# Kernel optimization log

Hardware: AMD Instinct MI355X
Metric: run time of the kernel (lower is better)

## Reference

```python
import jax, jax.numpy as jnp
import numpy as np

N, MA, F, NF = 512, 64, 128, 16
UPDATE_RATIO = 0.1
DECAY = 1.0
EPS = 1e-12  # avoids NaN grad of sqrt at self-distance 0 (torch diagonal is masked out by exp anyway)


def setup_inputs() -> dict:
    key = jax.random.key(0)
    ks = jax.random.split(key, 8)
    z = jax.random.randint(ks[0], (N, MA), 0, 10, dtype=jnp.int64) if jax.config.jax_enable_x64 else jax.random.randint(ks[0], (N, MA), 0, 10, dtype=jnp.int32)
    # pad last few atoms of each molecule with -1 to exercise the mask
    z = z.at[:, MA - 8:].set(-1)
    r = jax.random.normal(ks[1], (N, MA, 3), dtype=jnp.float32) * 3.0
    h = jax.random.normal(ks[2], (N, MA, F), dtype=jnp.float32)
    distances = jnp.linspace(0.5, 6.0, NF, dtype=jnp.float32)
    widths = jax.random.uniform(ks[3], (NF,), dtype=jnp.float32) * 0.5 + 0.5  # keep sigma > 0
    din = F * (1 + NF)  # 2176
    W1 = jax.random.normal(ks[4], (din, 512), dtype=jnp.float32) * (1.0 / np.sqrt(din))
    b1 = jnp.zeros((512,), dtype=jnp.float32)
    W2 = jax.random.normal(ks[5], (512, F), dtype=jnp.float32) * (1.0 / np.sqrt(512.0))
    b2 = jnp.zeros((F,), dtype=jnp.float32)
    return {"z": z, "r": r, "h": h, "distances": distances, "widths": widths,
            "W1": W1, "b1": b1, "W2": W2, "b2": b2}


def reference(z, r, h, distances, widths, W1, b1, W2, b2):
    n, ma = z.shape
    nf = distances.shape[0]
    # pairwise distance: (n, ma, ma)
    dv = r[:, :, None, :] - r[:, None, :, :]
    d = jnp.sqrt(jnp.sum(dv * dv, axis=-1) + EPS)
    mu = distances.reshape(1, nf, 1, 1)
    sigma = widths.reshape(1, nf, 1, 1)
    mask1 = (z > -1).astype(h.dtype)                      # (n, ma)
    pair_mask = mask1[:, :, None] * mask1[:, None, :]     # (n, ma, ma)
    # Gaussian RBF scores, masked: (n, nf, ma, ma)
    w = pair_mask[:, None] * jnp.exp(-((d[:, None] - mu) ** 2) / sigma) * 5.0
    # aggregate neighbor features: (n, ma, nf, F) -> (n, ma, nf*F)
    u = jnp.einsum('nfab,nbc->nafc', w, h).reshape(n, ma, nf * h.shape[-1])
    v = jnp.concatenate([h, u], axis=2)                   # (n, ma, F*(1+nf))
    v = jax.nn.silu(v @ W1 + b1) @ W2 + b2                # MLP 'net'
    h_new = h + v * UPDATE_RATIO * DECAY * mask1[:, :, None]
    return (z, r, h_new)
```

## Files before the change

### kernel.cpp

```cpp
#include <hip/hip_runtime.h>

#define MA 64
#define F 128
#define NF 16
#define HID 512
#define LDUB 144
#define LDWB 144
#define LDT1B 1040
#define UB0 0
#define UB1 9216
#define WL0 18432
#define WL1 27648

typedef float  float4v __attribute__((ext_vector_type(4)));
typedef short  short8  __attribute__((ext_vector_type(8)));
typedef int    int8v   __attribute__((ext_vector_type(8)));

static __device__ __forceinline__ unsigned int pack2bf(float x, float y) {
    unsigned int a = __float_as_uint(x) + 0x8000u;
    unsigned int b = __float_as_uint(y) + 0x8000u;
    return __builtin_amdgcn_perm(b, a, 0x07060302u);
}
static __device__ __forceinline__ unsigned short f2bf1(float x) {
    return (unsigned short)((__float_as_uint(x) + 0x8000u) >> 16);
}
static __device__ __forceinline__ unsigned int pk4fp8(float a, float b, float c, float d) {
    int p = __builtin_amdgcn_cvt_pk_fp8_f32(a, b, 0, false);
    p = __builtin_amdgcn_cvt_pk_fp8_f32(c, d, p, true);
    return (unsigned int)p;
}

#define LGKM_BAR() do {                                        \
    asm volatile("s_waitcnt lgkmcnt(0)" ::: "memory");         \
    __builtin_amdgcn_s_barrier();                              \
    asm volatile("" ::: "memory");                             \
} while (0)

__global__ void pack_frags(const float* __restrict__ W1, const float* __restrict__ W2,
                           unsigned char* __restrict__ w1p, unsigned short* __restrict__ w2p) {
    int gid  = blockIdx.x * 4 + (threadIdx.x >> 6);
    int lane = threadIdx.x & 63;
    int arow = lane & 15;
    int kq   = lane >> 4;
    if (gid < 544) {
        int kt = gid >> 5, jt = gid & 31;
        const float* base = W1 + (size_t)(kt * 128 + kq * 32) * HID + jt * 16 + arow;
        unsigned int o[8];
        #pragma unroll
        for (int p = 0; p < 8; p++)
            o[p] = pk4fp8(base[(p * 4 + 0) * HID], base[(p * 4 + 1) * HID],
                          base[(p * 4 + 2) * HID], base[(p * 4 + 3) * HID]);
        unsigned char* dst = w1p + ((size_t)gid * 64 + lane) * 32;
        *(uint4*)dst        = (uint4){o[0], o[1], o[2], o[3]};
        *(uint4*)(dst + 16) = (uint4){o[4], o[5], o[6], o[7]};
    } else if (gid < 544 + 128) {
        int g2 = gid - 544;
        int kt = g2 >> 3, mt = g2 & 7;
        const float* base = W2 + (size_t)(kt * 32 + kq * 8) * F + mt * 16 + arow;
        short8 o;
        #pragma unroll
        for (int j = 0; j < 8; j++) o[j] = (short)f2bf1(base[j * F]);
        *(short8*)(w2p + ((size_t)g2 * 64 + lane) * 8) = o;
    }
}

__launch_bounds__(512, 4)
__global__ void node_conv_mfma(const int* __restrict__ z, const float* __restrict__ rr,
        const float* __restrict__ h, const float* __restrict__ dist,
        const float* __restrict__ wid, const float* __restrict__ b1,
        const float* __restrict__ b2,
        const unsigned char* __restrict__ w1p, const unsigned short* __restrict__ w2p,
        float* __restrict__ out) {
    const int n = blockIdx.x;
    const int tid = threadIdx.x;
    const int lane = tid & 63;
    const int wave = tid >> 6;
    const int arow = lane & 15;
    const int quad = lane >> 4;
    const int kgrp = quad * 8;

    __shared__ __attribute__((aligned(16))) unsigned char lds[66560];
    __shared__ float r_lds[MA][5];

    const int N = gridDim.x;
    const float* hg = h + (size_t)n * MA * F;

    if (tid < MA) {
        int zi = z[n * MA + tid];
        out[(size_t)n * MA + tid] = (float)zi;
        r_lds[tid][0] = rr[(n * MA + tid) * 3 + 0];
        r_lds[tid][1] = rr[(n * MA + tid) * 3 + 1];
        r_lds[tid][2] = rr[(n * MA + tid) * 3 + 2];
        r_lds[tid][3] = (zi > -1) ? 1.0f : 0.0f;
    }
    if (tid < MA * 3)
        out[(size_t)N * MA + (size_t)n * MA * 3 + tid] = rr[(size_t)n * MA * 3 + tid];

    for (int i = tid; i < MA * F / 4; i += 512) {
        float4 v = ((const float4*)hg)[i];
        int a = i >> 5, c4 = (i & 31) * 4;
        *(unsigned int*)&lds[UB0 + a * LDUB + c4] = pk4fp8(v.x, v.y, v.z, v.w);
    }
    short8 ah[2];
    {
        int c = wave * 16 + arow;
        #pragma unroll
        for (int ks2 = 0; ks2 < 2; ks2++)
            #pragma unroll
            for (int j = 0; j < 8; j++)
                ah[ks2][j] = (short)f2bf1(hg[(size_t)(ks2 * 32 + kgrp + j) * F + c]);
    }
    __syncthreads();

    const int wa = tid >> 3;
    const int wb0 = (tid & 7) * 8;
    float dpre[8];
    {
        float ax = r_lds[wa][0], ay = r_lds[wa][1], az = r_lds[wa][2];
        float am = r_lds[wa][3];
        #pragma unroll
        for (int j = 0; j < 8; j++) {
            float dx = ax - r_lds[wb0 + j][0];
            float dy = ay - r_lds[wb0 + j][1];
            float dz = az - r_lds[wb0 + j][2];
            float d = sqrtf(dx * dx + dy * dy + dz * dz + 1e-12f);
            float mm = am * r_lds[wb0 + j][3];
            dpre[j] = d + (1.0f - mm) * 1e4f;
        }
    }

    {
        float mu = dist[0];
        float isg = 1.0f / wid[0];
        float e[8];
        #pragma unroll
        for (int j = 0; j < 8; j++) {
            float t = dpre[j] - mu;
            e[j] = 5.0f * __expf(-t * t * isg);
        }
        uint4 wp = { pack2bf(e[0], e[1]), pack2bf(e[2], e[3]),
                     pack2bf(e[4], e[5]), pack2bf(e[6], e[7]) };
        *(uint4*)&lds[WL0 + wa * LDWB + wb0 * 2] = wp;
    }
    int8v afrA, afrB;
    {
        const unsigned char* p0 = w1p + ((size_t)((wave * 4) * 64 + lane)) * 32;
        afrA = *(const int8v*)p0;
        afrB = *(const int8v*)(p0 + 2048);
    }
    LGKM_BAR();

    const float4v zf = {0.f, 0.f, 0.f, 0.f};
    float4v acc[4][4];
    #pragma unroll
    for (int i = 0; i < 4; i++)
        #pragma unroll
        for (int jv = 0; jv < 4; jv++) acc[i][jv] = zf;

    for (int f = 0; f <= NF; f++) {
        const int sel = f & 1;
        const int ubR = sel ? UB1 : UB0;
        const int ubW = sel ? UB0 : UB1;
        const int wlR = sel ? WL1 : WL0;
        const int wlW = sel ? WL0 : WL1;
        const unsigned char* pseg = w1p + ((size_t)((f * 32 + wave * 4) * 64 + lane)) * 32;

        #pragma unroll
        for (int at = 0; at < 4; at++) {
            int8v bfr = *(const int8v*)&lds[ubR + (at * 16 + arow) * LDUB + quad * 32];
            acc[0][at] = __builtin_amdgcn_mfma_scale_f32_16x16x128_f8f6f4(
                afrA, bfr, acc[0][at], 0, 0, 0, 127, 0, 127);
            acc[1][at] = __builtin_amdgcn_mfma_scale_f32_16x16x128_f8f6f4(
                afrB, bfr, acc[1][at], 0, 0, 0, 127, 0, 127);
        }
        afrA = *(const int8v*)(pseg + 2 * 2048);
        afrB = *(const int8v*)(pseg + 3 * 2048);
        #pragma unroll
        for (int at = 0; at < 4; at++) {
            int8v bfr = *(const int8v*)&lds[ubR + (at * 16 + arow) * LDUB + quad * 32];
            acc[2][at] = __builtin_amdgcn_mfma_scale_f32_16x16x128_f8f6f4(
                afrA, bfr, acc[2][at], 0, 0, 0, 127, 0, 127);
            acc[3][at] = __builtin_amdgcn_mfma_scale_f32_16x16x128_f8f6f4(
                afrB, bfr, acc[3][at], 0, 0, 0, 127, 0, 127);
        }

        if (f < NF) {
            const unsigned char* pN = w1p + ((size_t)(((f + 1) * 32 + wave * 4) * 64 + lane)) * 32;
            afrA = *(const int8v*)pN;
            afrB = *(const int8v*)(pN + 2048);

            #pragma unroll
            for (int atp = 0; atp < 2; atp++) {
                float4v ud0 = zf, ud1 = zf;
                #pragma unroll
                for (int ks2 = 0; ks2 < 2; ks2++) {
                    short8 bw0 = *(const short8*)&lds[wlR + ((atp * 2 + 0) * 16 + arow) * LDWB + (ks2 * 32 + kgrp) * 2];
                    ud0 = __builtin_amdgcn_mfma_f32_16x16x32_bf16(ah[ks2], bw0, ud0, 0, 0, 0);
                    short8 bw1 = *(const short8*)&lds[wlR + ((atp * 2 + 1) * 16 + arow) * LDWB + (ks2 * 32 + kgrp) * 2];
                    ud1 = __builtin_amdgcn_mfma_f32_16x16x32_bf16(ah[ks2], bw1, ud1, 0, 0, 0);
                }
                unsigned int u0 = pk4fp8(ud0[0], ud0[1], ud0[2], ud0[3]);
                unsigned int u1 = pk4fp8(ud1[0], ud1[1], ud1[2], ud1[3]);
                *(unsigned int*)&lds[ubW + ((atp * 2 + 0) * 16 + arow) * LDUB + wave * 16 + quad * 4] = u0;
                *(unsigned int*)&lds[ubW + ((atp * 2 + 1) * 16 + arow) * LDUB + wave * 16 + quad * 4] = u1;
            }

            if (f <= NF - 2) {
                float mu = dist[f + 1];
                float isg = 1.0f / wid[f + 1];
                float e[8];
                #pragma unroll
                for (int j = 0; j < 8; j++) {
                    float t = dpre[j] - mu;
                    e[j] = 5.0f * __expf(-t * t * isg);
                }
                uint4 wp = { pack2bf(e[0], e[1]), pack2bf(e[2], e[3]),
                             pack2bf(e[4], e[5]), pack2bf(e[6], e[7]) };
                *(uint4*)&lds[wlW + wa * LDWB + wb0 * 2] = wp;
            }
        }
        LGKM_BAR();
    }

    float4 b1v[4];
    #pragma unroll
    for (int mt = 0; mt < 4; mt++)
        b1v[mt] = *(const float4*)&b1[wave * 64 + mt * 16 + quad * 4];

    #pragma unroll
    for (int mt = 0; mt < 4; mt++) {
        #pragma unroll
        for (int at = 0; at < 4; at++) {
            float xs[4];
            #pragma unroll
            for (int r = 0; r < 4; r++) {
                float x = acc[mt][at][r] + ((const float*)&b1v[mt])[r];
                xs[r] = x / (1.0f + __expf(-x));
            }
            uint2 pv = { pack2bf(xs[0], xs[1]), pack2bf(xs[2], xs[3]) };
            *(uint2*)&lds[(at * 16 + arow) * LDT1B + (wave * 64 + mt * 16 + quad * 4) * 2] = pv;
        }
    }
    LGKM_BAR();

    float4v g2[4];
    #pragma unroll
    for (int n2 = 0; n2 < 4; n2++) g2[n2] = zf;

    short8 awA = *(const short8*)(w2p + ((size_t)(wave) * 64 + lane) * 8);
    #pragma unroll
    for (int ks2 = 0; ks2 < 8; ks2++) {
        const int k1 = 2 * ks2 + 1;
        short8 awB = *(const short8*)(w2p + ((size_t)(k1 * 8 + wave) * 64 + lane) * 8);
        #pragma unroll
        for (int n2 = 0; n2 < 4; n2++) {
            short8 bt = *(const short8*)&lds[(n2 * 16 + arow) * LDT1B + ((2 * ks2) * 32 + kgrp) * 2];
            g2[n2] = __builtin_amdgcn_mfma_f32_16x16x32_bf16(awA, bt, g2[n2], 0, 0, 0);
        }
        const int k2 = (ks2 < 7) ? 2 * ks2 + 2 : 0;
        awA = *(const short8*)(w2p + ((size_t)(k2 * 8 + wave) * 64 + lane) * 8);
        #pragma unroll
        for (int n2 = 0; n2 < 4; n2++) {
            short8 bt = *(const short8*)&lds[(n2 * 16 + arow) * LDT1B + ((2 * ks2 + 1) * 32 + kgrp) * 2];
            g2[n2] = __builtin_amdgcn_mfma_f32_16x16x32_bf16(awB, bt, g2[n2], 0, 0, 0);
        }
    }

    float* outh = out + (size_t)N * MA * 4 + (size_t)n * MA * F;
    const int c0 = wave * 16 + quad * 4;
    float4 b2v = *(const float4*)&b2[c0];
    #pragma unroll
    for (int n2 = 0; n2 < 4; n2++) {
        int a = n2 * 16 + arow;
        float m = r_lds[a][3] * 0.1f;
        float4 hv = *(const float4*)&hg[a * F + c0];
        float4 res;
        res.x = hv.x + (g2[n2][0] + b2v.x) * m;
        res.y = hv.y + (g2[n2][1] + b2v.y) * m;
        res.z = hv.z + (g2[n2][2] + b2v.z) * m;
        res.w = hv.w + (g2[n2][3] + b2v.w) * m;
        *(float4*)&outh[(size_t)a * F + c0] = res;
    }
}

extern "C" void kernel_launch(void* const* d_in, const int* in_sizes, int n_in,
                              void* d_out, int out_size, void* d_ws, size_t ws_size,
                              hipStream_t stream) {
    const int*   z    = (const int*)d_in[0];
    const float* rr   = (const float*)d_in[1];
    const float* h    = (const float*)d_in[2];
    const float* dist = (const float*)d_in[3];
    const float* wid  = (const float*)d_in[4];
    const float* W1   = (const float*)d_in[5];
    const float* b1   = (const float*)d_in[6];
    const float* W2   = (const float*)d_in[7];
    const float* b2   = (const float*)d_in[8];
    float* out = (float*)d_out;

    int Nmol = in_sizes[0] / MA;

    unsigned char*  w1p = (unsigned char*)d_ws;
    unsigned short* w2p = (unsigned short*)(w1p + (size_t)544 * 64 * 32);

    pack_frags<<<168, 256, 0, stream>>>(W1, W2, w1p, w2p);
    node_conv_mfma<<<Nmol, 512, 0, stream>>>(z, rr, h, dist, wid, b1, b2, w1p, w2p, out);
}
```

Baseline: 174.6 us.

## Double block to 1024 threads, splitting per-wave MFMA work in half

Launches 16 waves per molecule instead of 8. Each wave now owns half as many hidden-unit tiles in the first GEMM and half the atom rows in the RBF aggregation and second GEMM, and the RBF weight computation is spread over more threads. The aim is more latency hiding and fewer accumulator registers per wave. In exchange, blocks per CU may drop because of the LDS limit (about 66KB per block), and more waves contend at every barrier.

New measurement: 144.6 us. 1.21x faster.

```diff
diff --git a/kernel.cpp b/kernel.cpp
--- a/kernel.cpp
+++ b/kernel.cpp
@@ -64,7 +64,7 @@
     }
 }
 
-__launch_bounds__(512, 4)
+__launch_bounds__(1024, 4)
 __global__ void node_conv_mfma(const int* __restrict__ z, const float* __restrict__ rr,
         const float* __restrict__ h, const float* __restrict__ dist,
         const float* __restrict__ wid, const float* __restrict__ b1,
@@ -78,6 +78,8 @@
     const int arow = lane & 15;
     const int quad = lane >> 4;
     const int kgrp = quad * 8;
+    const int whi = wave >> 1;
+    const int wlo = wave & 1;
 
     __shared__ __attribute__((aligned(16))) unsigned char lds[66560];
     __shared__ float r_lds[MA][5];
@@ -96,14 +98,14 @@
     if (tid < MA * 3)
         out[(size_t)N * MA + (size_t)n * MA * 3 + tid] = rr[(size_t)n * MA * 3 + tid];
 
-    for (int i = tid; i < MA * F / 4; i += 512) {
+    for (int i = tid; i < MA * F / 4; i += 1024) {
         float4 v = ((const float4*)hg)[i];
         int a = i >> 5, c4 = (i & 31) * 4;
         *(unsigned int*)&lds[UB0 + a * LDUB + c4] = pk4fp8(v.x, v.y, v.z, v.w);
     }
     short8 ah[2];
     {
-        int c = wave * 16 + arow;
+        int c = whi * 16 + arow;
         #pragma unroll
         for (int ks2 = 0; ks2 < 2; ks2++)
             #pragma unroll
@@ -112,14 +114,14 @@
     }
     __syncthreads();
 
-    const int wa = tid >> 3;
-    const int wb0 = (tid & 7) * 8;
-    float dpre[8];
+    const int wa = tid >> 4;
+    const int wb0 = (tid & 15) * 4;
+    float dpre[4];
     {
         float ax = r_lds[wa][0], ay = r_lds[wa][1], az = r_lds[wa][2];
         float am = r_lds[wa][3];
         #pragma unroll
-        for (int j = 0; j < 8; j++) {
+        for (int j = 0; j < 4; j++) {
             float dx = ax - r_lds[wb0 + j][0];
             float dy = ay - r_lds[wb0 + j][1];
             float dz = az - r_lds[wb0 + j][2];
@@ -132,28 +134,27 @@
     {
         float mu = dist[0];
         float isg = 1.0f / wid[0];
-        float e[8];
-        #pragma unroll
-        for (int j = 0; j < 8; j++) {
+        float e[4];
+        #pragma unroll
+        for (int j = 0; j < 4; j++) {
             float t = dpre[j] - mu;
             e[j] = 5.0f * __expf(-t * t * isg);
         }
-        uint4 wp = { pack2bf(e[0], e[1]), pack2bf(e[2], e[3]),
-                     pack2bf(e[4], e[5]), pack2bf(e[6], e[7]) };
-        *(uint4*)&lds[WL0 + wa * LDWB + wb0 * 2] = wp;
-    }
-    int8v afrA, afrB;
-    {
-        const unsigned char* p0 = w1p + ((size_t)((wave * 4) * 64 + lane)) * 32;
-        afrA = *(const int8v*)p0;
-        afrB = *(const int8v*)(p0 + 2048);
+        uint2 wp = { pack2bf(e[0], e[1]), pack2bf(e[2], e[3]) };
+        *(uint2*)&lds[WL0 + wa * LDWB + wb0 * 2] = wp;
+    }
+    int8v afr[2];
+    {
+        const unsigned char* p0 = w1p + ((size_t)((wave * 2) * 64 + lane)) * 32;
+        afr[0] = *(const int8v*)p0;
+        afr[1] = *(const int8v*)(p0 + 2048);
     }
     LGKM_BAR();
 
     const float4v zf = {0.f, 0.f, 0.f, 0.f};
-    float4v acc[4][4];
-    #pragma unroll
-    for (int i = 0; i < 4; i++)
+    float4v acc[2][4];
+    #pragma unroll
+    for (int i = 0; i < 2; i++)
         #pragma unroll
         for (int jv = 0; jv < 4; jv++) acc[i][jv] = zf;
 
@@ -163,72 +164,57 @@
         const int ubW = sel ? UB0 : UB1;
         const int wlR = sel ? WL1 : WL0;
         const int wlW = sel ? WL0 : WL1;
-        const unsigned char* pseg = w1p + ((size_t)((f * 32 + wave * 4) * 64 + lane)) * 32;
 
         #pragma unroll
         for (int at = 0; at < 4; at++) {
             int8v bfr = *(const int8v*)&lds[ubR + (at * 16 + arow) * LDUB + quad * 32];
             acc[0][at] = __builtin_amdgcn_mfma_scale_f32_16x16x128_f8f6f4(
-                afrA, bfr, acc[0][at], 0, 0, 0, 127, 0, 127);
+                afr[0], bfr, acc[0][at], 0, 0, 0, 127, 0, 127);
             acc[1][at] = __builtin_amdgcn_mfma_scale_f32_16x16x128_f8f6f4(
-                afrB, bfr, acc[1][at], 0, 0, 0, 127, 0, 127);
-        }
-        afrA = *(const int8v*)(pseg + 2 * 2048);
-        afrB = *(const int8v*)(pseg + 3 * 2048);
-        #pragma unroll
-        for (int at = 0; at < 4; at++) {
-            int8v bfr = *(const int8v*)&lds[ubR + (at * 16 + arow) * LDUB + quad * 32];
-            acc[2][at] = __builtin_amdgcn_mfma_scale_f32_16x16x128_f8f6f4(
-                afrA, bfr, acc[2][at], 0, 0, 0, 127, 0, 127);
-            acc[3][at] = __builtin_amdgcn_mfma_scale_f32_16x16x128_f8f6f4(
-                afrB, bfr, acc[3][at], 0, 0, 0, 127, 0, 127);
+                afr[1], bfr, acc[1][at], 0, 0, 0, 127, 0, 127);
         }
 
         if (f < NF) {
-            const unsigned char* pN = w1p + ((size_t)(((f + 1) * 32 + wave * 4) * 64 + lane)) * 32;
-            afrA = *(const int8v*)pN;
-            afrB = *(const int8v*)(pN + 2048);
-
+            const unsigned char* pN = w1p + ((size_t)(((f + 1) * 32 + wave * 2) * 64 + lane)) * 32;
+            afr[0] = *(const int8v*)pN;
+            afr[1] = *(const int8v*)(pN + 2048);
+
+            float4v ud0 = zf, ud1 = zf;
             #pragma unroll
-            for (int atp = 0; atp < 2; atp++) {
-                float4v ud0 = zf, ud1 = zf;
-                #pragma unroll
-                for (int ks2 = 0; ks2 < 2; ks2++) {
-                    short8 bw0 = *(const short8*)&lds[wlR + ((atp * 2 + 0) * 16 + arow) * LDWB + (ks2 * 32 + kgrp) * 2];
-                    ud0 = __builtin_amdgcn_mfma_f32_16x16x32_bf16(ah[ks2], bw0, ud0, 0, 0, 0);
-                    short8 bw1 = *(const short8*)&lds[wlR + ((atp * 2 + 1) * 16 + arow) * LDWB + (ks2 * 32 + kgrp) * 2];
-                    ud1 = __builtin_amdgcn_mfma_f32_16x16x32_bf16(ah[ks2], bw1, ud1, 0, 0, 0);
-                }
-                unsigned int u0 = pk4fp8(ud0[0], ud0[1], ud0[2], ud0[3]);
-                unsigned int u1 = pk4fp8(ud1[0], ud1[1], ud1[2], ud1[3]);
-                *(unsigned int*)&lds[ubW + ((atp * 2 + 0) * 16 + arow) * LDUB + wave * 16 + quad * 4] = u0;
-                *(unsigned int*)&lds[ubW + ((atp * 2 + 1) * 16 + arow) * LDUB + wave * 16 + quad * 4] = u1;
+            for (int ks2 = 0; ks2 < 2; ks2++) {
+                short8 bw0 = *(const short8*)&lds[wlR + ((wlo * 2 + 0) * 16 + arow) * LDWB + (ks2 * 32 + kgrp) * 2];
+                ud0 = __builtin_amdgcn_mfma_f32_16x16x32_bf16(ah[ks2], bw0, ud0, 0, 0, 0);
+                short8 bw1 = *(const short8*)&lds[wlR + ((wlo * 2 + 1) * 16 + arow) * LDWB + (ks2 * 32 + kgrp) * 2];
+                ud1 = __builtin_amdgcn_mfma_f32_16x16x32_bf16(ah[ks2], bw1, ud1, 0, 0, 0);
             }
+            unsigned int u0 = pk4fp8(ud0[0], ud0[1], ud0[2], ud0[3]);
+            unsigned int u1 = pk4fp8(ud1[0], ud1[1], ud1[2], ud1[3]);
+            *(unsigned int*)&lds[ubW + ((wlo * 2 + 0) * 16 + arow) * LDUB + whi * 16 + quad * 4] = u0;
+            *(unsigned int*)&lds[ubW + ((wlo * 2 + 1) * 16 + arow) * LDUB + whi * 16 + quad * 4] = u1;
 
             if (f <= NF - 2) {
                 float mu = dist[f + 1];
                 float isg = 1.0f / wid[f + 1];
-                float e[8];
+                float e[4];
                 #pragma unroll
-                for (int j = 0; j < 8; j++) {
+                for (int j = 0; j < 4; j++) {
                     float t = dpre[j] - mu;
                     e[j] = 5.0f * __expf(-t * t * isg);
                 }
-                uint4 wp = { pack2bf(e[0], e[1]), pack2bf(e[2], e[3]),
-                             pack2bf(e[4], e[5]), pack2bf(e[6], e[7]) };
-                *(uint4*)&lds[wlW + wa * LDWB + wb0 * 2] = wp;
+                uint2 wp = { pack2bf(e[0], e[1]), pack2bf(e[2], e[3]) };
+                *(uint2*)&lds[wlW + wa * LDWB + wb0 * 2] = wp;
             }
         }
         LGKM_BAR();
     }
 
-    float4 b1v[4];
-    #pragma unroll
-    for (int mt = 0; mt < 4; mt++)
-        b1v[mt] = *(const float4*)&b1[wave * 64 + mt * 16 + quad * 4];
-
-    #pragma unroll
-    for (int mt = 0; mt < 4; mt++) {
+    float4 b1v[2];
+    #pragma unroll
+    for (int mt = 0; mt < 2; mt++)
+        b1v[mt] = *(const float4*)&b1[wave * 32 + mt * 16 + quad * 4];
+
+    #pragma unroll
+    for (int mt = 0; mt < 2; mt++) {
         #pragma unroll
         for (int at = 0; at < 4; at++) {
             float xs[4];
@@ -238,47 +224,45 @@
                 xs[r] = x / (1.0f + __expf(-x));
             }
             uint2 pv = { pack2bf(xs[0], xs[1]), pack2bf(xs[2], xs[3]) };
-            *(uint2*)&lds[(at * 16 + arow) * LDT1B + (wave * 64 + mt * 16 + quad * 4) * 2] = pv;
+            *(uint2*)&lds[(at * 16 + arow) * LDT1B + (wave * 32 + mt * 16 + quad * 4) * 2] = pv;
         }
     }
     LGKM_BAR();
 
-    float4v g2[4];
-    #pragma unroll
-    for (int n2 = 0; n2 < 4; n2++) g2[n2] = zf;
-
-    short8 awA = *(const short8*)(w2p + ((size_t)(wave) * 64 + lane) * 8);
+    float4v g2[2] = { zf, zf };
+
+    short8 awA = *(const short8*)(w2p + ((size_t)(whi) * 64 + lane) * 8);
     #pragma unroll
     for (int ks2 = 0; ks2 < 8; ks2++) {
         const int k1 = 2 * ks2 + 1;
-        short8 awB = *(const short8*)(w2p + ((size_t)(k1 * 8 + wave) * 64 + lane) * 8);
-        #pragma unroll
-        for (int n2 = 0; n2 < 4; n2++) {
-            short8 bt = *(const short8*)&lds[(n2 * 16 + arow) * LDT1B + ((2 * ks2) * 32 + kgrp) * 2];
-            g2[n2] = __builtin_amdgcn_mfma_f32_16x16x32_bf16(awA, bt, g2[n2], 0, 0, 0);
+        short8 awB = *(const short8*)(w2p + ((size_t)(k1 * 8 + whi) * 64 + lane) * 8);
+        #pragma unroll
+        for (int j = 0; j < 2; j++) {
+            short8 bt = *(const short8*)&lds[((wlo * 2 + j) * 16 + arow) * LDT1B + ((2 * ks2) * 32 + kgrp) * 2];
+            g2[j] = __builtin_amdgcn_mfma_f32_16x16x32_bf16(awA, bt, g2[j], 0, 0, 0);
         }
         const int k2 = (ks2 < 7) ? 2 * ks2 + 2 : 0;
-        awA = *(const short8*)(w2p + ((size_t)(k2 * 8 + wave) * 64 + lane) * 8);
-        #pragma unroll
-        for (int n2 = 0; n2 < 4; n2++) {
-            short8 bt = *(const short8*)&lds[(n2 * 16 + arow) * LDT1B + ((2 * ks2 + 1) * 32 + kgrp) * 2];
-            g2[n2] = __builtin_amdgcn_mfma_f32_16x16x32_bf16(awB, bt, g2[n2], 0, 0, 0);
+        awA = *(const short8*)(w2p + ((size_t)(k2 * 8 + whi) * 64 + lane) * 8);
+        #pragma unroll
+        for (int j = 0; j < 2; j++) {
+            short8 bt = *(const short8*)&lds[((wlo * 2 + j) * 16 + arow) * LDT1B + ((2 * ks2 + 1) * 32 + kgrp) * 2];
+            g2[j] = __builtin_amdgcn_mfma_f32_16x16x32_bf16(awB, bt, g2[j], 0, 0, 0);
         }
     }
 
     float* outh = out + (size_t)N * MA * 4 + (size_t)n * MA * F;
-    const int c0 = wave * 16 + quad * 4;
+    const int c0 = whi * 16 + quad * 4;
     float4 b2v = *(const float4*)&b2[c0];
     #pragma unroll
-    for (int n2 = 0; n2 < 4; n2++) {
-        int a = n2 * 16 + arow;
+    for (int j = 0; j < 2; j++) {
+        int a = (wlo * 2 + j) * 16 + arow;
         float m = r_lds[a][3] * 0.1f;
         float4 hv = *(const float4*)&hg[a * F + c0];
         float4 res;
-        res.x = hv.x + (g2[n2][0] + b2v.x) * m;
-        res.y = hv.y + (g2[n2][1] + b2v.y) * m;
-        res.z = hv.z + (g2[n2][2] + b2v.z) * m;
-        res.w = hv.w + (g2[n2][3] + b2v.w) * m;
+        res.x = hv.x + (g2[j][0] + b2v.x) * m;
+        res.y = hv.y + (g2[j][1] + b2v.y) * m;
+        res.z = hv.z + (g2[j][2] + b2v.z) * m;
+        res.w = hv.w + (g2[j][3] + b2v.w) * m;
         *(float4*)&outh[(size_t)a * F + c0] = res;
     }
 }
@@ -303,5 +287,5 @@
     unsigned short* w2p = (unsigned short*)(w1p + (size_t)544 * 64 * 32);
 
     pack_frags<<<168, 256, 0, stream>>>(W1, W2, w1p, w2p);
-    node_conv_mfma<<<Nmol, 512, 0, stream>>>(z, rr, h, dist, wid, b1, b2, w1p, w2p, out);
-}
+    node_conv_mfma<<<Nmol, 1024, 0, stream>>>(z, rr, h, dist, wid, b1, b2, w1p, w2p, out);
+}
```
